# Optimization experiments

Hardware: AMD Instinct MI355X
Metric: run time of the kernel (lower is better)

The kernel has to match this reference:

```python
import jax, jax.numpy as jnp
import numpy as np

INPUT_SIZE = 64
HIDDEN = 512
BATCH = 256
SEQ = 512

def _rnn_layer(x, W_ih, W_hh, b_ih, b_hh):
    # x: (B, T, D_in). PyTorch RNN step: h_t = tanh(x_t W_ih^T + b_ih + h_{t-1} W_hh^T + b_hh)
    B = x.shape[0]
    # precompute input projections for all timesteps: (B, T, H)
    xp = jnp.einsum('btd,hd->bth', x, W_ih) + b_ih + b_hh
    h0 = jnp.zeros((B, W_hh.shape[0]), dtype=x.dtype)

    def step(h, xp_t):
        h_new = jnp.tanh(xp_t + h @ W_hh.T)
        return h_new, h_new

    _, hs = jax.lax.scan(step, h0, jnp.swapaxes(xp, 0, 1))  # hs: (T, B, H)
    return jnp.swapaxes(hs, 0, 1)  # (B, T, H)

def setup_inputs() -> dict:
    key = jax.random.key(0)
    ks = jax.random.split(key, 11)
    s_in = 1.0 / np.sqrt(HIDDEN)
    u = lambda k, shape: jax.random.uniform(k, shape, jnp.float32, -s_in, s_in)
    return {
        'x': jax.random.normal(ks[0], (BATCH, SEQ, INPUT_SIZE), jnp.float32),
        'W_ih0': u(ks[1], (HIDDEN, INPUT_SIZE)),
        'W_hh0': u(ks[2], (HIDDEN, HIDDEN)),
        'b_ih0': u(ks[3], (HIDDEN,)),
        'b_hh0': u(ks[4], (HIDDEN,)),
        'W_ih1': u(ks[5], (HIDDEN, HIDDEN)),
        'W_hh1': u(ks[6], (HIDDEN, HIDDEN)),
        'b_ih1': u(ks[7], (HIDDEN,)),
        'b_hh1': u(ks[8], (HIDDEN,)),
        'W_fc': u(ks[9], (1, HIDDEN)),
        'b_fc': u(ks[10], (1,)),
    }

def reference(x, W_ih0, W_hh0, b_ih0, b_hh0, W_ih1, W_hh1, b_ih1, b_hh1, W_fc, b_fc):
    h1 = _rnn_layer(x, W_ih0, W_hh0, b_ih0, b_hh0)   # (B, T, H)
    h2 = _rnn_layer(h1, W_ih1, W_hh1, b_ih1, b_hh1)  # (B, T, H)
    last = h2[:, -1, :]                              # (B, H)
    return last @ W_fc.T + b_fc                      # (B, 1)
```

## Files before the change

### kernel.cpp

```cpp
#include <hip/hip_runtime.h>
#include <hip/hip_fp16.h>


typedef _Float16 h8 __attribute__((ext_vector_type(8)));
typedef float    f4 __attribute__((ext_vector_type(4)));

#define HID   512
#define TSEQ  512
#define NB    256
#define NW    4
#define NAGF  64
#define NVGF  40
#define NREGF (NAGF + NVGF)
#define NLDSF 24

#define MFMA_A(accv, av, bv) \
  asm("v_mfma_f32_16x16x32_f16 %0, %1, %2, %0" : "+v"(accv) : "v"(av), "a"(bv))
#define MFMA_V(accv, av, bv) \
  asm("v_mfma_f32_16x16x32_f16 %0, %1, %2, %0" : "+v"(accv) : "v"(av), "v"(bv))

#if __has_builtin(__builtin_amdgcn_rcpf)
#define FAST_RCP(x) __builtin_amdgcn_rcpf(x)
#else
#define FAST_RCP(x) (1.0f / (x))
#endif

static const size_t OFF_P   = 0;
static const size_t OFF_B0  = 134217728;
static const size_t OFF_B1  = OFF_B0 + 65536;
static const size_t OFF_R0  = OFF_B1 + 524288;
static const size_t OFF_L0  = OFF_R0 + 425984;
static const size_t OFF_R1  = OFF_L0 + 98304;
static const size_t OFF_L1  = OFF_R1 + 425984;
static const size_t OFF_BS0 = OFF_L1 + 98304;
static const size_t OFF_BS1 = OFF_BS0 + 2048;

__global__ void bias_kernel(const float* __restrict__ bih0, const float* __restrict__ bhh0,
                            const float* __restrict__ bih1, const float* __restrict__ bhh1,
                            float* __restrict__ bias0, float* __restrict__ bias1) {
  int i = threadIdx.x;
  bias0[i] = bih0[i] + bhh0[i];
  bias1[i] = bih1[i] + bhh1[i];
}

__global__ void cvt_half_kernel(const float* __restrict__ in, _Float16* __restrict__ outp, int n) {
  int i = blockIdx.x * 256 + threadIdx.x;
  if (i < n) outp[i] = (_Float16)in[i];
}

__global__ void pack_rec_kernel(const float* __restrict__ W, uint4* __restrict__ BregP,
                                uint4* __restrict__ BldsP) {
  int t = blockIdx.x * 256 + threadIdx.x;
  int l  = t & 63;
  int g  = (t >> 6) & 7;
  int kk = (t >> 9) & 15;
  int w  = (t >> 13) & 3;
  int n  = 128 * w + 16 * g + (l & 15);
  int k0 = 32 * kk + ((l >> 4) & 3) * 8;
  const float* src = W + (size_t)n * HID + k0;
  h8 v;
#pragma unroll
  for (int i = 0; i < 8; ++i) v[i] = (_Float16)src[i];
  uint4 u = __builtin_bit_cast(uint4, v);
  if (g < 4) {
    BregP[(w * NREGF + 4 * kk + g) * 64 + l] = u;
  } else if (g == 4) {
    BregP[(w * NREGF + NAGF + kk) * 64 + l] = u;
  } else if (g == 5) {
    BregP[(w * NREGF + NAGF + 16 + kk) * 64 + l] = u;
  } else if (g == 6) {
    if (kk < 8) BregP[(w * NREGF + NAGF + 32 + kk) * 64 + l] = u;
    else        BldsP[(w * NLDSF + (kk - 8)) * 64 + l] = u;
  } else {
    BldsP[(w * NLDSF + 8 + kk) * 64 + l] = u;
  }
}

template <typename AT, int K>
__global__ __launch_bounds__(256, 2) void proj_kernel(const AT* A, const _Float16* __restrict__ Bw,
                                                      _Float16* C, const float* __restrict__ bias) {
  __shared__ _Float16 At[64][40];
  __shared__ _Float16 Bt[512][40];
  const int tid = threadIdx.x;
  const int m0 = blockIdx.x * 64;
  const int wv = tid >> 6;
  const int l = tid & 63;
  const int n0 = wv * 128;
  const int lm = l & 15;
  const int lq = l >> 4;

  f4 acc[4][8];
#pragma unroll
  for (int i = 0; i < 4; ++i)
#pragma unroll
    for (int j = 0; j < 8; ++j) acc[i][j] = (f4){0.f, 0.f, 0.f, 0.f};

  const int arow = tid >> 2;
  const int kq = (tid & 3) * 8;

  for (int k0 = 0; k0 < K; k0 += 32) {
    if (sizeof(AT) == 4) {
      const float* ap = (const float*)A + (size_t)(m0 + arow) * K + k0 + kq;
      h8 v;
#pragma unroll
      for (int i = 0; i < 8; ++i) v[i] = (_Float16)ap[i];
      *(h8*)&At[arow][kq] = v;
    } else {
      *(h8*)&At[arow][kq] = *(const h8*)((const _Float16*)A + (size_t)(m0 + arow) * K + k0 + kq);
    }
#pragma unroll
    for (int rr = 0; rr < 8; ++rr) {
      int rrow = arow + rr * 64;
      *(h8*)&Bt[rrow][kq] = *(const h8*)(Bw + (size_t)rrow * K + k0 + kq);
    }
    __syncthreads();
    h8 af[4];
#pragma unroll
    for (int mm = 0; mm < 4; ++mm) af[mm] = *(const h8*)&At[mm * 16 + lm][lq * 8];
#pragma unroll
    for (int nn = 0; nn < 8; ++nn) {
      h8 bf = *(const h8*)&Bt[n0 + nn * 16 + lm][lq * 8];
#pragma unroll
      for (int mm = 0; mm < 4; ++mm)
        acc[mm][nn] = __builtin_amdgcn_mfma_f32_16x16x32_f16(af[mm], bf, acc[mm][nn], 0, 0, 0);
    }
    __syncthreads();
  }
#pragma unroll
  for (int nn = 0; nn < 8; ++nn) {
    int col = n0 + nn * 16 + lm;
    float bv = bias[col];
#pragma unroll
    for (int mm = 0; mm < 4; ++mm) {
#pragma unroll
      for (int r = 0; r < 4; ++r) {
        int row = m0 + mm * 16 + lq * 4 + r;
        C[(size_t)row * HID + col] = (_Float16)(acc[mm][nn][r] + bv);
      }
    }
  }
}

template <bool WRITE_H, bool DO_FC>
__global__ __launch_bounds__(256, 1) void rec_kernel(
    const _Float16* __restrict__ P, _Float16* __restrict__ Pout,
    const uint4* __restrict__ BregP, const uint4* __restrict__ BldsP,
    const float* __restrict__ Wfc, const float* __restrict__ bfc, float* __restrict__ out) {
  __shared__ __align__(16) uint4 Blds[NW * NLDSF * 64];
  __shared__ __align__(16) _Float16 hbuf[2][HID];
  __shared__ float red[NW];
  const int tid = threadIdx.x;
  const int b = blockIdx.x;
  const int w = tid >> 6, l = tid & 63, lq = l >> 4, lm = l & 15;

  h8 breg_a[NAGF];
#pragma unroll
  for (int i = 0; i < NAGF; ++i)
    breg_a[i] = __builtin_bit_cast(h8, BregP[(w * NREGF + i) * 64 + l]);
  h8 breg_v[NVGF];
#pragma unroll
  for (int i = 0; i < NVGF; ++i)
    breg_v[i] = __builtin_bit_cast(h8, BregP[(w * NREGF + NAGF + i) * 64 + l]);
#pragma unroll
  for (int j = 0; j < NLDSF; ++j)
    Blds[(w * NLDSF + j) * 64 + l] = BldsP[(w * NLDSF + j) * 64 + l];

  ((unsigned int*)hbuf)[tid] = 0;
  __syncthreads();

  const int col1 = 128 * w + 16 * lq + lm;
  const int col2 = col1 + 64;

  const _Float16* prow = P + (size_t)b * TSEQ * HID;
  unsigned short xp1c = *(const unsigned short*)(prow + col1);
  unsigned short xp2c = *(const unsigned short*)(prow + col2);
  float lv1 = 0.f, lv2 = 0.f;

#pragma unroll 1
  for (int t = 0; t < TSEQ; ++t) {
    int tn = (t + 1 < TSEQ) ? t + 1 : t;
    unsigned short xp1n = *(const unsigned short*)(prow + (size_t)tn * HID + col1);
    unsigned short xp2n = *(const unsigned short*)(prow + (size_t)tn * HID + col2);
    const _Float16* hb = hbuf[t & 1];

    f4 acc[8];
#pragma unroll
    for (int g = 0; g < 8; ++g) acc[g] = (f4){0.f, 0.f, 0.f, 0.f};

#pragma unroll
    for (int kk = 0; kk < 16; ++kk) {
      h8 a = *(const h8*)(hb + kk * 32 + lq * 8);
      MFMA_A(acc[0], a, breg_a[4 * kk + 0]);
      MFMA_A(acc[1], a, breg_a[4 * kk + 1]);
      MFMA_A(acc[2], a, breg_a[4 * kk + 2]);
      MFMA_A(acc[3], a, breg_a[4 * kk + 3]);
      MFMA_V(acc[4], a, breg_v[kk]);
      MFMA_V(acc[5], a, breg_v[16 + kk]);
      if (kk < 8) {
        MFMA_V(acc[6], a, breg_v[32 + kk]);
      } else {
        h8 bf = __builtin_bit_cast(h8, Blds[(w * NLDSF + (kk - 8)) * 64 + l]);
        MFMA_V(acc[6], a, bf);
      }
      {
        h8 bf = __builtin_bit_cast(h8, Blds[(w * NLDSF + 8 + kk) * 64 + l]);
        MFMA_V(acc[7], a, bf);
      }
    }

    float hr1 = (lq == 0) ? acc[0][0]
              : (lq == 1) ? acc[1][0]
              : (lq == 2) ? acc[2][0]
                          : acc[3][0];
    float hr2 = (lq == 0) ? acc[4][0]
              : (lq == 1) ? acc[5][0]
              : (lq == 2) ? acc[6][0]
                          : acc[7][0];

    float s1 = hr1 + (float)__builtin_bit_cast(_Float16, xp1c);
    float s2 = hr2 + (float)__builtin_bit_cast(_Float16, xp2c);
    float e1 = __expf(2.0f * s1);
    float e2 = __expf(2.0f * s2);
    float v1 = 1.0f - 2.0f * FAST_RCP(e1 + 1.0f);
    float v2 = 1.0f - 2.0f * FAST_RCP(e2 + 1.0f);
    lv1 = v1; lv2 = v2;
    _Float16 hw1 = (_Float16)v1, hw2 = (_Float16)v2;
    _Float16* hn = hbuf[(t + 1) & 1];
    hn[col1] = hw1;
    hn[col2] = hw2;
    if (WRITE_H) {
      _Float16* po = Pout + (size_t)b * TSEQ * HID + (size_t)t * HID;
      po[col1] = hw1;
      po[col2] = hw2;
    }
    __syncthreads();
    xp1c = xp1n; xp2c = xp2n;
  }

  if (DO_FC) {
    float fc = lv1 * Wfc[col1] + lv2 * Wfc[col2];
#pragma unroll
    for (int off = 32; off; off >>= 1) fc += __shfl_down(fc, off, 64);
    if (l == 0) red[w] = fc;
    __syncthreads();
    if (tid == 0) {
      float s = bfc[0];
#pragma unroll
      for (int i = 0; i < NW; ++i) s += red[i];
      out[b] = s;
    }
  }
}

extern "C" void kernel_launch(void* const* d_in, const int* in_sizes, int n_in,
                              void* d_out, int out_size, void* d_ws, size_t ws_size,
                              hipStream_t stream) {
  const float* x    = (const float*)d_in[0];
  const float* Wih0 = (const float*)d_in[1];
  const float* Whh0 = (const float*)d_in[2];
  const float* bih0 = (const float*)d_in[3];
  const float* bhh0 = (const float*)d_in[4];
  const float* Wih1 = (const float*)d_in[5];
  const float* Whh1 = (const float*)d_in[6];
  const float* bih1 = (const float*)d_in[7];
  const float* bhh1 = (const float*)d_in[8];
  const float* Wfc  = (const float*)d_in[9];
  const float* bfc  = (const float*)d_in[10];
  float* out = (float*)d_out;
  char* ws = (char*)d_ws;

  _Float16* P  = (_Float16*)(ws + OFF_P);
  _Float16* B0 = (_Float16*)(ws + OFF_B0);
  _Float16* B1 = (_Float16*)(ws + OFF_B1);
  uint4* R0 = (uint4*)(ws + OFF_R0);
  uint4* L0 = (uint4*)(ws + OFF_L0);
  uint4* R1 = (uint4*)(ws + OFF_R1);
  uint4* L1 = (uint4*)(ws + OFF_L1);
  float* bias0 = (float*)(ws + OFF_BS0);
  float* bias1 = (float*)(ws + OFF_BS1);

  bias_kernel<<<1, 512, 0, stream>>>(bih0, bhh0, bih1, bhh1, bias0, bias1);
  cvt_half_kernel<<<128, 256, 0, stream>>>(Wih0, B0, 512 * 64);
  cvt_half_kernel<<<1024, 256, 0, stream>>>(Wih1, B1, 512 * 512);
  pack_rec_kernel<<<128, 256, 0, stream>>>(Whh0, R0, L0);
  pack_rec_kernel<<<128, 256, 0, stream>>>(Whh1, R1, L1);

  proj_kernel<float, 64><<<2048, 256, 0, stream>>>(x, B0, P, bias0);
  rec_kernel<true, false><<<NB, 256, 0, stream>>>(P, P, R0, L0, nullptr, nullptr, nullptr);
  proj_kernel<_Float16, 512><<<2048, 256, 0, stream>>>(P, B1, P, bias1);
  rec_kernel<false, true><<<NB, 256, 0, stream>>>(P, nullptr, R1, L1, Wfc, bfc, out);
}
```

Baseline: 1.659 ms.

## Software-pipeline LDS weight and hidden-state loads one k-step ahead of MFMAs

```diff
diff --git a/kernel.cpp b/kernel.cpp
--- a/kernel.cpp
+++ b/kernel.cpp
@@ -10,9 +10,9 @@
 #define NB    256
 #define NW    4
 #define NAGF  64
-#define NVGF  40
+#define NVGF  34
 #define NREGF (NAGF + NVGF)
-#define NLDSF 24
+#define NLDSF 30
 
 #define MFMA_A(accv, av, bv) \
   asm("v_mfma_f32_16x16x32_f16 %0, %1, %2, %0" : "+v"(accv) : "v"(av), "a"(bv))
@@ -29,10 +29,10 @@
 static const size_t OFF_B0  = 134217728;
 static const size_t OFF_B1  = OFF_B0 + 65536;
 static const size_t OFF_R0  = OFF_B1 + 524288;
-static const size_t OFF_L0  = OFF_R0 + 425984;
-static const size_t OFF_R1  = OFF_L0 + 98304;
-static const size_t OFF_L1  = OFF_R1 + 425984;
-static const size_t OFF_BS0 = OFF_L1 + 98304;
+static const size_t OFF_L0  = OFF_R0 + 401408;
+static const size_t OFF_R1  = OFF_L0 + 122880;
+static const size_t OFF_L1  = OFF_R1 + 401408;
+static const size_t OFF_BS0 = OFF_L1 + 122880;
 static const size_t OFF_BS1 = OFF_BS0 + 2048;
 
 __global__ void bias_kernel(const float* __restrict__ bih0, const float* __restrict__ bhh0,
@@ -69,10 +69,10 @@
   } else if (g == 5) {
     BregP[(w * NREGF + NAGF + 16 + kk) * 64 + l] = u;
   } else if (g == 6) {
-    if (kk < 8) BregP[(w * NREGF + NAGF + 32 + kk) * 64 + l] = u;
-    else        BldsP[(w * NLDSF + (kk - 8)) * 64 + l] = u;
+    if (kk < 2) BregP[(w * NREGF + NAGF + 32 + kk) * 64 + l] = u;
+    else        BldsP[(w * NLDSF + (kk - 2)) * 64 + l] = u;
   } else {
-    BldsP[(w * NLDSF + 8 + kk) * 64 + l] = u;
+    BldsP[(w * NLDSF + 14 + kk) * 64 + l] = u;
   }
 }
 
@@ -176,6 +176,8 @@
   unsigned short xp2c = *(const unsigned short*)(prow + col2);
   float lv1 = 0.f, lv2 = 0.f;
 
+  h8 b7carry = __builtin_bit_cast(h8, Blds[(w * NLDSF + 14) * 64 + l]);
+
 #pragma unroll 1
   for (int t = 0; t < TSEQ; ++t) {
     int tn = (t + 1 < TSEQ) ? t + 1 : t;
@@ -187,26 +189,33 @@
 #pragma unroll
     for (int g = 0; g < 8; ++g) acc[g] = (f4){0.f, 0.f, 0.f, 0.f};
 
+    h8 aC = *(const h8*)(hb + lq * 8);
+    h8 b7C = b7carry;
+    h8 b6C = b7C;
+
 #pragma unroll
     for (int kk = 0; kk < 16; ++kk) {
-      h8 a = *(const h8*)(hb + kk * 32 + lq * 8);
-      MFMA_A(acc[0], a, breg_a[4 * kk + 0]);
-      MFMA_A(acc[1], a, breg_a[4 * kk + 1]);
-      MFMA_A(acc[2], a, breg_a[4 * kk + 2]);
-      MFMA_A(acc[3], a, breg_a[4 * kk + 3]);
-      MFMA_V(acc[4], a, breg_v[kk]);
-      MFMA_V(acc[5], a, breg_v[16 + kk]);
-      if (kk < 8) {
-        MFMA_V(acc[6], a, breg_v[32 + kk]);
+      h8 aN = aC, b6N = b6C, b7N = b7C;
+      if (kk < 15) {
+        aN  = *(const h8*)(hb + (kk + 1) * 32 + lq * 8);
+        b7N = __builtin_bit_cast(h8, Blds[(w * NLDSF + 14 + (kk + 1)) * 64 + l]);
+        if (kk + 1 >= 2)
+          b6N = __builtin_bit_cast(h8, Blds[(w * NLDSF + (kk + 1 - 2)) * 64 + l]);
       } else {
-        h8 bf = __builtin_bit_cast(h8, Blds[(w * NLDSF + (kk - 8)) * 64 + l]);
-        MFMA_V(acc[6], a, bf);
+        b7N = __builtin_bit_cast(h8, Blds[(w * NLDSF + 14) * 64 + l]);
       }
-      {
-        h8 bf = __builtin_bit_cast(h8, Blds[(w * NLDSF + 8 + kk) * 64 + l]);
-        MFMA_V(acc[7], a, bf);
-      }
-    }
+      MFMA_A(acc[0], aC, breg_a[4 * kk + 0]);
+      MFMA_A(acc[1], aC, breg_a[4 * kk + 1]);
+      MFMA_A(acc[2], aC, breg_a[4 * kk + 2]);
+      MFMA_A(acc[3], aC, breg_a[4 * kk + 3]);
+      MFMA_V(acc[4], aC, breg_v[kk]);
+      MFMA_V(acc[5], aC, breg_v[16 + kk]);
+      if (kk < 2) { MFMA_V(acc[6], aC, breg_v[32 + kk]); }
+      else        { MFMA_V(acc[6], aC, b6C); }
+      MFMA_V(acc[7], aC, b7C);
+      aC = aN; b6C = b6N; b7C = b7N;
+    }
+    b7carry = b7C;
 
     float hr1 = (lq == 0) ? acc[0][0]
               : (lq == 1) ? acc[1][0]
```

Measured after the change: 1.613 ms. -2.8%, faster.
